# Optimization experiments

Hardware: AMD Instinct MI355X
Metric: run time of the kernel (lower is better)

Reference implementation:

```python
import jax, jax.numpy as jnp
import numpy as np
import math

B, C, T = 4, 512, 2048
LN_EPS = 1e-5

def setup_inputs() -> dict:
    key = jax.random.key(0)
    ks = jax.random.split(key, 12)
    s = 1.0 / math.sqrt(C)
    inp = {
        'feat': jax.random.normal(ks[0], (B, C, T), dtype=jnp.float32),
        'Wq': jax.random.normal(ks[1], (C, C), dtype=jnp.float32) * s,
        'bq': jax.random.normal(ks[2], (C,), dtype=jnp.float32) * s,
        'Wk': jax.random.normal(ks[3], (C, C), dtype=jnp.float32) * s,
        'bk': jax.random.normal(ks[4], (C,), dtype=jnp.float32) * s,
        'Wv': jax.random.normal(ks[5], (C, C), dtype=jnp.float32) * s,
        'bv': jax.random.normal(ks[6], (C,), dtype=jnp.float32) * s,
        'Ws': jax.random.normal(ks[7], (C, C), dtype=jnp.float32) * s,
        'bs': jax.random.normal(ks[8], (C,), dtype=jnp.float32) * s,
        'Wl': jax.random.normal(ks[9], (C,), dtype=jnp.float32) * s,
        'bl': jax.random.normal(ks[10], (1,), dtype=jnp.float32) * s,
    }
    return inp

def reference(feat, Wq, bq, Wk, bk, Wv, bv, Ws, bs, Wl, bl):
    d = feat.shape[1]
    # 1x1 Conv1d == per-position linear over channels. feat: [B,C,T]
    value = jnp.einsum('oc,bct->bto', Wv, feat) + bv          # [B,T,C]
    query = jnp.einsum('oc,bct->bto', Wq, feat) + bq          # [B,T,C]
    key_  = jnp.einsum('oc,bct->bct', Wk, feat) + bk[:, None] # [B,C,T]
    f = jnp.einsum('btc,bcs->bts', query, key_) / math.sqrt(d)
    f = jax.nn.softmax(f, axis=2)                             # [B,T,T]
    y = jnp.einsum('bts,bsc->btc', f, value)                  # [B,T,C]
    f_score = jax.nn.sigmoid(jnp.einsum('btc,c->bt', y, Wl) + bl[0])
    z = jnp.einsum('bts,bsc->btc', 1.0 - f, value)            # [B,T,C]
    b_score = 1.0 - jax.nn.sigmoid(jnp.einsum('btc,c->bt', z, Wl) + bl[0])
    f_score = (f_score + b_score) / 2.0
    y_ct = jnp.einsum('oc,btc->bot', Ws, y) + bs[:, None]     # smooth conv, [B,C,T]
    out = feat + y_ct
    # LayerNorm over (C, T) jointly, default affine (weight=1, bias=0)
    mu = jnp.mean(out, axis=(1, 2), keepdims=True)
    var = jnp.mean(jnp.square(out - mu), axis=(1, 2), keepdims=True)
    out = (out - mu) * jax.lax.rsqrt(var + LN_EPS)
    return out, f_score
```

## Files before the change

### kernel.cpp

```cpp
#include <hip/hip_runtime.h>
#include <hip/hip_bf16.h>

#define BB 4
#define CC 512
#define TT 2048
static constexpr long CT  = (long)CC * TT;
static constexpr long TC  = (long)TT * CC;
static constexpr long TTT = (long)TT * TT;
static constexpr float SM_SCALE = 0.04419417382415922f;

typedef __bf16 bf16;
typedef __attribute__((ext_vector_type(8))) __bf16 bf16x8;
typedef __attribute__((ext_vector_type(4))) __bf16 bf16x4;
typedef __attribute__((ext_vector_type(4))) float f32x4;

__device__ __forceinline__ void load_lds16(const bf16* g, bf16* l)
{
    __builtin_amdgcn_global_load_lds(
        (const __attribute__((address_space(1))) void*)g,
        (__attribute__((address_space(3))) void*)l, 16, 0, 0);
}

template <int TM, int TN, int WR, int WC, int BK>
struct Core {
    static constexpr int THREADS = WR * WC * 64;
    static constexpr int MI = TM / (WR * 16);
    static constexpr int NI = TN / (WC * 16);
    static constexpr int CPR = BK / 8;
    static constexpr int RSH = (BK == 64) ? 3 : 2;
    static constexpr int CMASK = CPR - 1;
    static constexpr int CHUNKS = (TM + TN) * CPR;
    static constexpr int ACH = TM * CPR;
    static constexpr int CPT = CHUNKS / THREADS;
    static_assert(CPT * THREADS == CHUNKS, "chunk divisibility");

    __device__ static __forceinline__ void run(
        const bf16* __restrict__ Ab, const bf16* __restrict__ Bb,
        int K, int m0, int n0, bf16* As, bf16* Bs, f32x4 (&acc)[MI][NI])
    {
        const int tid  = threadIdx.x;
        const int lane = tid & 63;
        const int wid  = tid >> 6;
        const int wr = (wid / WC) * (MI * 16);
        const int wc = (wid % WC) * (NI * 16);
        const int lm = lane & 15;
        const int lq = lane >> 4;
        for (int k0 = 0; k0 < K; k0 += BK) {
#pragma unroll
            for (int i = 0; i < CPT; ++i) {
                int c = tid + i * THREADS;
                if (c < ACH) {
                    int row = c >> RSH;
                    int gc  = (c & CMASK) ^ (row & CMASK);
                    load_lds16(Ab + (long)(m0 + row) * K + k0 + gc * 8, As + c * 8);
                } else {
                    int d = c - ACH;
                    int row = d >> RSH;
                    int gc  = (d & CMASK) ^ (row & CMASK);
                    load_lds16(Bb + (long)(n0 + row) * K + k0 + gc * 8, Bs + d * 8);
                }
            }
            __syncthreads();
#pragma unroll
            for (int ks = 0; ks < BK / 32; ++ks) {
                bf16x8 af[MI], bfr[NI];
#pragma unroll
                for (int i = 0; i < MI; ++i) {
                    int ar = wr + i * 16 + lm;
                    int cc = (ks * 4 + lq) ^ (ar & CMASK);
                    af[i] = *(const bf16x8*)(As + ar * BK + cc * 8);
                }
#pragma unroll
                for (int i = 0; i < NI; ++i) {
                    int br = wc + i * 16 + lm;
                    int cc = (ks * 4 + lq) ^ (br & CMASK);
                    bfr[i] = *(const bf16x8*)(Bs + br * BK + cc * 8);
                }
#pragma unroll
                for (int mi = 0; mi < MI; ++mi)
#pragma unroll
                    for (int ni = 0; ni < NI; ++ni)
                        acc[mi][ni] = __builtin_amdgcn_mfma_f32_16x16x32_bf16(
                            af[mi], bfr[ni], acc[mi][ni], 0, 0, 0);
            }
            __syncthreads();
        }
    }
};

struct CoreQV {
    static constexpr int THREADS = 512;
    static constexpr int MI = 2;
    static constexpr int NI = 4;
    static constexpr int BK = 64;
    static constexpr int CPR = 8, RSH = 3, CMASK = 7;
    static constexpr int ACH = 128 * 8;
    static constexpr int CHUNKS = 256 * 8;
    static constexpr int CPT = CHUNKS / THREADS;

    __device__ static __forceinline__ void run(
        const bf16* __restrict__ Ab, const bf16* __restrict__ Bq,
        const bf16* __restrict__ Bv,
        int m0, bf16* As, bf16* Bs, f32x4 (&acc)[MI][NI])
    {
        const int tid  = threadIdx.x;
        const int lane = tid & 63;
        const int wid  = tid >> 6;
        const int wr = (wid / 2) * 32;
        const int wc = (wid % 2) * 64;
        const int lm = lane & 15;
        const int lq = lane >> 4;
        for (int k0 = 0; k0 < 512; k0 += BK) {
#pragma unroll
            for (int i = 0; i < CPT; ++i) {
                int c = tid + i * THREADS;
                if (c < ACH) {
                    int row = c >> RSH;
                    int gc  = (c & CMASK) ^ (row & CMASK);
                    load_lds16(Ab + (long)(m0 + row) * 512 + k0 + gc * 8, As + c * 8);
                } else {
                    int d = c - ACH;
                    int row = d >> RSH;
                    int gc  = (d & CMASK) ^ (row & CMASK);
                    const bf16* src = (row < 64)
                        ? Bq + (long)row * 512
                        : Bv + (long)(row - 64) * 512;
                    load_lds16(src + k0 + gc * 8, Bs + d * 8);
                }
            }
            __syncthreads();
#pragma unroll
            for (int ks = 0; ks < 2; ++ks) {
                bf16x8 af[MI], bfr[NI];
#pragma unroll
                for (int i = 0; i < MI; ++i) {
                    int ar = wr + i * 16 + lm;
                    int cc = (ks * 4 + lq) ^ (ar & CMASK);
                    af[i] = *(const bf16x8*)(As + ar * BK + cc * 8);
                }
#pragma unroll
                for (int i = 0; i < NI; ++i) {
                    int br = wc + i * 16 + lm;
                    int cc = (ks * 4 + lq) ^ (br & CMASK);
                    bfr[i] = *(const bf16x8*)(Bs + br * BK + cc * 8);
                }
#pragma unroll
                for (int mi = 0; mi < MI; ++mi)
#pragma unroll
                    for (int ni = 0; ni < NI; ++ni)
                        acc[mi][ni] = __builtin_amdgcn_mfma_f32_16x16x32_bf16(
                            af[mi], bfr[ni], acc[mi][ni], 0, 0, 0);
            }
            __syncthreads();
        }
    }
};

__global__ __launch_bounds__(512)
void gemm_qv_kernel(const bf16* __restrict__ featT, const bf16* __restrict__ Wq_bf,
                    const bf16* __restrict__ Wv_bf, bf16* __restrict__ Qb,
                    bf16* __restrict__ Vt, const float* __restrict__ bq,
                    const float* __restrict__ bv, const float* __restrict__ wkc,
                    const float* __restrict__ bk, float* __restrict__ qb)
{
    __shared__ bf16 As[128 * 64];
    __shared__ bf16 Bs[128 * 64];
    const int rb = blockIdx.z;
    const int m0 = blockIdx.y * 128;
    const int ng = blockIdx.x;
    const long wofs = (long)(ng * 64) * 512;
    f32x4 acc[2][4] = {};
    CoreQV::run(featT + (long)rb * TC, Wq_bf + wofs, Wv_bf + wofs, m0, As, Bs, acc);

    const int lane = threadIdx.x & 63, wid = threadIdx.x >> 6;
    const int wr = (wid / 2) * 32;
    const bool isV = wid & 1;
    const int lm = lane & 15, lq = lane >> 4;

    if (isV) {
        bf16* outV = Vt + (long)rb * CT;
#pragma unroll
        for (int mi = 0; mi < 2; ++mi)
#pragma unroll
            for (int ni = 0; ni < 4; ++ni) {
                int n = ng * 64 + ni * 16 + lm;
                float bn = bv[n];
                int mb = m0 + wr + mi * 16 + lq * 4;
                bf16x4 pk;
#pragma unroll
                for (int r = 0; r < 4; ++r) pk[r] = (bf16)(acc[mi][ni][r] + bn);
                *(bf16x4*)(outV + (long)n * TT + mb) = pk;
            }
    } else {
        bf16* out = Qb + (long)rb * TC;
        float* qbb = qb + (long)rb * TT;
        float rs[2][4] = {};
#pragma unroll
        for (int mi = 0; mi < 2; ++mi)
#pragma unroll
            for (int ni = 0; ni < 4; ++ni) {
                int n = ng * 64 + ni * 16 + lm;
                float bn = bq[n], wn = wkc[n], kn = bk[n];
#pragma unroll
                for (int r = 0; r < 4; ++r) {
                    int m = m0 + wr + mi * 16 + lq * 4 + r;
                    float v = acc[mi][ni][r] + bn;
                    rs[mi][r] += v * kn;
                    out[(long)m * 512 + n] = (bf16)(v * wn);
                }
            }
#pragma unroll
        for (int mi = 0; mi < 2; ++mi)
#pragma unroll
            for (int r = 0; r < 4; ++r) {
                float s = rs[mi][r];
                s += __shfl_xor(s, 1, 64); s += __shfl_xor(s, 2, 64);
                s += __shfl_xor(s, 4, 64); s += __shfl_xor(s, 8, 64);
                if (lm == 0)
                    atomicAdd(qbb + m0 + wr + mi * 16 + lq * 4 + r, s);
            }
    }
}

__global__ __launch_bounds__(512, 2)
void gemm_s256_kernel(const bf16* __restrict__ Qb, const bf16* __restrict__ featT,
                      bf16* __restrict__ S, const float* __restrict__ qb,
                      float* __restrict__ rsum)
{
    __shared__ __align__(16) bf16 lds[2][2][256 * 64];
    const int id   = blockIdx.x;
    const int xcd  = id & 7, sIdx = id >> 3;
    const int bz   = xcd >> 1;
    const int n0   = (sIdx & 7) * 256;
    const int m0   = (((xcd & 1) << 2) + (sIdx >> 3)) * 256;
    const bf16* __restrict__ Ab = Qb + (long)bz * TC;
    const bf16* __restrict__ Bb = featT + (long)bz * TC;

    const int tid  = threadIdx.x;
    const int lane = tid & 63;
    const int wid  = tid >> 6;
    const int lm = lane & 15, lq = lane >> 4;
    const int wrb = (wid >> 2) * 64;
    const int wcb = (wid & 3) * 32;

    f32x4 acc[8][4] = {};

#define FENCE asm volatile("" ::: "memory")

#define STAGE_HT(t, op, h)                                                    \
    do {                                                                      \
        const bf16* gp_ = (op) ? Bb : Ab;                                     \
        const int  br_  = ((op) ? n0 : m0) + (h) * 128;                       \
        bf16* lp_ = &lds[(t) & 1][op][(h) * 128 * 64];                        \
        _Pragma("unroll")                                                     \
        for (int i_ = 0; i_ < 2; ++i_) {                                      \
            int c_ = tid + i_ * 512;                                          \
            int r_ = c_ >> 3;                                                 \
            int g_ = (c_ & 7) ^ (r_ & 7);                                     \
            load_lds16(gp_ + (long)(br_ + r_) * 512 + (t) * 64 + g_ * 8,      \
                       lp_ + c_ * 8);                                         \
        }                                                                     \
    } while (0)

#define PHASE(t, qm, qn, doSt, st, sop, sh, doVm)                             \
    do {                                                                      \
        bf16x8 af[2][4], bfr[2][2];                                           \
        const bf16* Al_ = lds[(t) & 1][0];                                    \
        const bf16* Bl_ = lds[(t) & 1][1];                                    \
        _Pragma("unroll")                                                     \
        for (int ks = 0; ks < 2; ++ks) {                                      \
            _Pragma("unroll")                                                 \
            for (int j = 0; j < 4; ++j) {                                     \
                int ar = (qm) * 128 + wrb + j * 16 + lm;                      \
                int cc = (ks * 4 + lq) ^ (ar & 7);                            \
                af[ks][j] = *(const bf16x8*)(Al_ + ar * 64 + cc * 8);         \
            }                                                                 \
            _Pragma("unroll")                                                 \
            for (int j = 0; j < 2; ++j) {                                     \
                int br = (qn) * 128 + wcb + j * 16 + lm;                      \
                int cc = (ks * 4 + lq) ^ (br & 7);                            \
                bfr[ks][j] = *(const bf16x8*)(Bl_ + br * 64 + cc * 8);        \
            }                                                                 \
        }                                                                     \
        if (doSt) STAGE_HT(st, sop, sh);                                      \
        if (doVm) {                                                           \
            if ((t) < 6) asm volatile("s_waitcnt vmcnt(4)" ::: "memory");     \
            else         asm volatile("s_waitcnt vmcnt(0)" ::: "memory");     \
        }                                                                     \
        FENCE; __builtin_amdgcn_s_barrier(); FENCE;                           \
        __builtin_amdgcn_s_setprio(1);                                        \
        _Pragma("unroll")                                                     \
        for (int ks = 0; ks < 2; ++ks)                                        \
            _Pragma("unroll")                                                 \
            for (int j = 0; j < 4; ++j)                                       \
                _Pragma("unroll")                                             \
                for (int j2 = 0; j2 < 2; ++j2)                                \
                    acc[(qm) * 4 + j][(qn) * 2 + j2] =                        \
                        __builtin_amdgcn_mfma_f32_16x16x32_bf16(              \
                            af[ks][j], bfr[ks][j2],                           \
                            acc[(qm) * 4 + j][(qn) * 2 + j2], 0, 0, 0);       \
        __builtin_amdgcn_s_setprio(0);                                        \
        FENCE; __builtin_amdgcn_s_barrier(); FENCE;                           \
    } while (0)

    STAGE_HT(0, 0, 0); STAGE_HT(0, 1, 0); STAGE_HT(0, 0, 1); STAGE_HT(0, 1, 1);
    STAGE_HT(1, 0, 0); STAGE_HT(1, 1, 0);
    asm volatile("s_waitcnt vmcnt(4)" ::: "memory");
    FENCE; __builtin_amdgcn_s_barrier(); FENCE;

    for (int t = 0; t < 8; ++t) {
        PHASE(t, 0, 0, t + 1 < 8, t + 1, 0, 1, false);
        PHASE(t, 0, 1, t + 1 < 8, t + 1, 1, 1, false);
        PHASE(t, 1, 0, t + 2 < 8, t + 2, 0, 0, false);
        PHASE(t, 1, 1, t + 2 < 8, t + 2, 1, 0, true);
    }
#undef PHASE
#undef STAGE_HT
#undef FENCE

    bf16* outp = S + (long)bz * TTT;
    const float* qbb = qb + (long)bz * TT;
    float* rsb = rsum + (long)bz * TT;
#pragma unroll
    for (int mi = 0; mi < 8; ++mi) {
        const int mrow = m0 + (mi >> 2) * 128 + wrb + (mi & 3) * 16 + lq * 4;
        const f32x4 qv = *(const f32x4*)(qbb + mrow);
        float rp[4] = {0.f, 0.f, 0.f, 0.f};
#pragma unroll
        for (int ni = 0; ni < 4; ++ni) {
            const int ncol = n0 + (ni >> 1) * 128 + wcb + (ni & 1) * 16 + lm;
#pragma unroll
            for (int r = 0; r < 4; ++r) {
                float p = __expf((acc[mi][ni][r] + qv[r]) * SM_SCALE);
                outp[(long)(mrow + r) * 2048 + ncol] = (bf16)p;
                rp[r] += p;
            }
        }
#pragma unroll
        for (int r = 0; r < 4; ++r) {
            float s2 = rp[r];
            s2 += __shfl_xor(s2, 1, 64); s2 += __shfl_xor(s2, 2, 64);
            s2 += __shfl_xor(s2, 4, 64); s2 += __shfl_xor(s2, 8, 64);
            if (lm == 0) atomicAdd(rsb + mrow + r, s2);
        }
    }
}

using CY = Core<128, 64, 4, 2, 64>;
__global__ __launch_bounds__(512)
void gemm_y_kernel(const bf16* __restrict__ S, const bf16* __restrict__ Vt,
                   bf16* __restrict__ Yb, const float* __restrict__ Wl,
                   const float* __restrict__ rsum, float* __restrict__ u)
{
    __shared__ bf16 As[128 * 64];
    __shared__ bf16 Bs[64 * 64];
    const int id = blockIdx.x;
    const int xcd = id & 7, s = id >> 3;
    const int rb = xcd >> 1;
    const int n0 = (s & 7) * 64;
    const int m0 = (((xcd & 1) << 3) + (s >> 3)) * 128;
    f32x4 acc[CY::MI][CY::NI] = {};
    CY::run(S + (long)rb * TTT, Vt + (long)rb * CT, 2048, m0, n0, As, Bs, acc);

    const int lane = threadIdx.x & 63, wid = threadIdx.x >> 6;
    const int wr = (wid / 2) * 32, wc = (wid % 2) * 32;
    const int lm = lane & 15, lq = lane >> 4;
    bf16* out = Yb + (long)rb * TC;
    const float* rsb = rsum + (long)rb * TT;
    float* ub = u + (long)rb * TT;
    float inv[2][4];
#pragma unroll
    for (int mi = 0; mi < 2; ++mi)
#pragma unroll
        for (int r = 0; r < 4; ++r)
            inv[mi][r] = 1.f / rsb[m0 + wr + mi * 16 + lq * 4 + r];
    float rs[2][4] = {};
#pragma unroll
    for (int mi = 0; mi < 2; ++mi)
#pragma unroll
        for (int ni = 0; ni < 2; ++ni) {
            int n = n0 + wc + ni * 16 + lm;
            float wn = Wl[n];
#pragma unroll
            for (int r = 0; r < 4; ++r) {
                int m = m0 + wr + mi * 16 + lq * 4 + r;
                float v = acc[mi][ni][r] * inv[mi][r];
                out[(long)m * 512 + n] = (bf16)v;
                rs[mi][r] += v * wn;
            }
        }
#pragma unroll
    for (int mi = 0; mi < 2; ++mi)
#pragma unroll
        for (int r = 0; r < 4; ++r) {
            float s2 = rs[mi][r];
            s2 += __shfl_xor(s2, 1, 64); s2 += __shfl_xor(s2, 2, 64);
            s2 += __shfl_xor(s2, 4, 64); s2 += __shfl_xor(s2, 8, 64);
            if (lm == 0)
                atomicAdd(ub + m0 + wr + mi * 16 + lq * 4 + r, s2);
        }
}

using CF = Core<128, 64, 4, 2, 64>;
__global__ __launch_bounds__(512)
void gemm_final_kernel(const bf16* __restrict__ Yb, const bf16* __restrict__ Ws_bf,
                       float* __restrict__ out, const float* __restrict__ bs,
                       const float* __restrict__ feat, double* __restrict__ stats)
{
    __shared__ bf16 As[128 * 64];
    __shared__ bf16 Bs[64 * 64];
    __shared__ float red[16];
    const int id = blockIdx.x;
    const int xcd = id & 7, s = id >> 3;
    const int bz = xcd >> 1;
    const int n0 = (s & 7) * 64;
    const int m0 = (((xcd & 1) << 3) + (s >> 3)) * 128;
    f32x4 acc[CF::MI][CF::NI] = {};
    CF::run(Yb + (long)bz * TC, Ws_bf, 512, m0, n0, As, Bs, acc);

    const int tid = threadIdx.x;
    const int lane = tid & 63, wid = tid >> 6;
    const int wr = (wid / 2) * 32, wc = (wid % 2) * 32;
    const int lm = lane & 15, lq = lane >> 4;
    float s1 = 0.f, s2 = 0.f;
#pragma unroll
    for (int mi = 0; mi < 2; ++mi)
#pragma unroll
        for (int ni = 0; ni < 2; ++ni) {
            int mbase = m0 + wr + mi * 16 + lq * 4;
            int n = n0 + wc + ni * 16 + lm;
            long off = (long)bz * CT + (long)n * TT + mbase;
            f32x4 fv = *(const f32x4*)(feat + off);
            float bn = bs[n];
            f32x4 res;
#pragma unroll
            for (int r = 0; r < 4; ++r) {
                float v = acc[mi][ni][r] + bn + fv[r];
                res[r] = v;
                s1 += v;
                s2 += v * v;
            }
            *(f32x4*)(out + off) = res;
        }
#pragma unroll
    for (int off = 32; off; off >>= 1) {
        s1 += __shfl_xor(s1, off, 64);
        s2 += __shfl_xor(s2, off, 64);
    }
    if (lane == 0) { red[wid] = s1; red[8 + wid] = s2; }
    __syncthreads();
    if (tid == 0) {
        double t1 = 0.0, t2 = 0.0;
#pragma unroll
        for (int w = 0; w < 8; ++w) { t1 += red[w]; t2 += red[8 + w]; }
        atomicAdd(stats + bz * 2, t1);
        atomicAdd(stats + bz * 2 + 1, t2);
    }
}

__global__ __launch_bounds__(256)
void prep_kernel(const float* __restrict__ feat, bf16* __restrict__ featT,
                 const float* __restrict__ Wq, const float* __restrict__ Wv,
                 const float* __restrict__ Ws, bf16* __restrict__ Wbf,
                 const float* __restrict__ Wk, const float* __restrict__ Wl,
                 const float* __restrict__ bv, float* __restrict__ wkc,
                 float* __restrict__ wvl, float* __restrict__ wlbv,
                 float* __restrict__ frp, float* __restrict__ qb,
                 float* __restrict__ u, float* __restrict__ rsum,
                 double* __restrict__ stats)
{
    const int blk = blockIdx.x;
    const int tid = threadIdx.x;
    if (blk < 4096) {
        __shared__ float tile[32][33];
        __shared__ float sfr[4][32];
        const int b  = blk >> 10;
        const int c0 = ((blk & 1023) >> 6) * 32;
        const int tt = blk & 63;
        const int t0 = tt * 32;
        const int tx = tid & 31;
        const int ty = tid >> 5;
#pragma unroll
        for (int j = 0; j < 4; ++j) {
            int c = c0 + ty + j * 8;
            tile[ty + j * 8][tx] = feat[(long)b * CT + (long)c * TT + t0 + tx];
        }
        __syncthreads();
        float ps = 0.f;
#pragma unroll
        for (int j = 0; j < 4; ++j) {
            int tl = ty + j * 8;
            int t = t0 + tl;
            int c = c0 + tx;
            float v = tile[tx][tl];
            ps += v;
            featT[(long)b * TC + (long)t * CC + c] = (bf16)v;
        }
        const int wid = tid >> 6;
        ps += __shfl_xor(ps, 32, 64);
        if ((tid & 63) < 32) sfr[wid][tx] = ps;
        __syncthreads();
        if (tid < 32) {
            float s = sfr[0][tid] + sfr[1][tid] + sfr[2][tid] + sfr[3][tid];
            frp[(((long)b * 64 + tt) << 9) + c0 + tid] = s;
        }
    } else if (blk < 4480) {
        long gid = (long)(blk - 4096) * 256 + tid;
        long idx = gid * 8;
        int w = (int)(idx >> 18);
        long off = idx & 262143;
        const float* src = (w == 0) ? Wq : (w == 1) ? Wv : Ws;
        f32x4 a = *(const f32x4*)(src + off);
        f32x4 b = *(const f32x4*)(src + off + 4);
        bf16x8 o;
#pragma unroll
        for (int j = 0; j < 4; ++j) { o[j] = (bf16)a[j]; o[4 + j] = (bf16)b[j]; }
        *(bf16x8*)(Wbf + idx) = o;
    } else {
        int mid = (blk - 4480) * 256 + tid;
        if (mid < 512) {
            float s = 0.f;
            for (int o = 0; o < 512; ++o) s += Wk[o * 512 + mid];
            wkc[mid] = s;
        } else if (mid < 1024) {
            int k = mid - 512;
            float s = 0.f;
            for (int c = 0; c < 512; ++c) s += Wl[c] * Wv[c * 512 + k];
            wvl[k] = s;
        } else if (mid < 1088) {
            int lane = mid - 1024;
            float s = 0.f;
#pragma unroll
            for (int j = 0; j < 8; ++j) s += Wl[lane + 64 * j] * bv[lane + 64 * j];
#pragma unroll
            for (int off = 32; off; off >>= 1) s += __shfl_xor(s, off, 64);
            if (lane == 0) wlbv[0] = s;
        } else if (mid >= 1152 && mid < 1160) {
            stats[mid - 1152] = 0.0;
        } else if (mid >= 4096 && mid < 12288) {
            qb[mid - 4096] = 0.f;
        } else if (mid >= 12288 && mid < 20480) {
            u[mid - 12288] = 0.f;
        } else if (mid >= 20480 && mid < 28672) {
            rsum[mid - 20480] = 0.f;
        }
    }
}

__global__ __launch_bounds__(256)
void ln_score_kernel(float* __restrict__ out, const double* __restrict__ stats,
                     const float* __restrict__ u, const float* __restrict__ frp,
                     const float* __restrict__ wvl, const float* __restrict__ wlbv,
                     const float* __restrict__ blp)
{
    if (blockIdx.x < 4096) {
        long i = ((long)blockIdx.x * 256 + threadIdx.x) * 4;
        int b = (int)(i >> 20);
        const double n = 1048576.0;
        double mu  = stats[b * 2] / n;
        double var = stats[b * 2 + 1] / n - mu * mu;
        float rs = (float)(1.0 / sqrt(var + 1e-5));
        float muf = (float)mu;
        f32x4 v = *(f32x4*)(out + i);
#pragma unroll
        for (int j = 0; j < 4; ++j) v[j] = (v[j] - muf) * rs;
        *(f32x4*)(out + i) = v;
    } else {
        const int b = blockIdx.x - 4096;
        __shared__ float ssv[4];
        const int tid = threadIdx.x, lane = tid & 63, wid = tid >> 6;
        const float* fb = frp + ((long)b * 64 << 9);
        float s0 = 0.f, s1 = 0.f;
#pragma unroll 8
        for (int k = 0; k < 64; ++k) {
            s0 += fb[(k << 9) + tid];
            s1 += fb[(k << 9) + tid + 256];
        }
        float p = s0 * wvl[tid] + s1 * wvl[tid + 256];
#pragma unroll
        for (int off = 32; off; off >>= 1) p += __shfl_xor(p, off, 64);
        if (lane == 0) ssv[wid] = p;
        __syncthreads();
        const float sv = ssv[0] + ssv[1] + ssv[2] + ssv[3] + 2048.f * wlbv[0];
        const float bl0 = blp[0];
#pragma unroll
        for (int j = 0; j < 8; ++j) {
            int t = tid + j * 256;
            float uu = u[(long)b * TT + t];
            float uf = uu + bl0;
            float vf = sv - uu + bl0;
            float fs  = 1.f / (1.f + __expf(-uf));
            float bsc = 1.f - 1.f / (1.f + __expf(-vf));
            out[(long)BB * CT + (long)b * TT + t] = 0.5f * (fs + bsc);
        }
    }
}

extern "C" void kernel_launch(void* const* d_in, const int* in_sizes, int n_in,
                              void* d_out, int out_size, void* d_ws, size_t ws_size,
                              hipStream_t stream)
{
    const float* feat = (const float*)d_in[0];
    const float* Wq   = (const float*)d_in[1];
    const float* bq   = (const float*)d_in[2];
    const float* Wk   = (const float*)d_in[3];
    const float* bk   = (const float*)d_in[4];
    const float* Wv   = (const float*)d_in[5];
    const float* bv   = (const float*)d_in[6];
    const float* Ws   = (const float*)d_in[7];
    const float* bs   = (const float*)d_in[8];
    const float* Wl   = (const float*)d_in[9];
    const float* bl   = (const float*)d_in[10];
    float* out = (float*)d_out;

    if (ws_size < 69316736) return;
    char* ws = (char*)d_ws;
    bf16* featT  = (bf16*)(ws);
    bf16* Wbf    = (bf16*)(ws + 8388608);
    bf16* Qb     = (bf16*)(ws + 9961472);
    bf16* Vt     = (bf16*)(ws + 18350080);
    bf16* Yb     = (bf16*)(ws + 26738688);
    bf16* S      = (bf16*)(ws + 35127296);
    float* wkc   = (float*)(ws + 68689920);
    float* wvl   = (float*)(ws + 68691968);
    float* wlbv  = (float*)(ws + 68694016);
    float* qb    = (float*)(ws + 68694080);
    double* stats= (double*)(ws + 68726848);
    float* u     = (float*)(ws + 68726912);
    float* rsum  = (float*)(ws + 68759680);
    float* frp   = (float*)(ws + 68792448);

    bf16* Wq_bf = Wbf;
    bf16* Wv_bf = Wbf + 262144;
    bf16* Ws_bf = Wbf + 524288;

    prep_kernel<<<4592, 256, 0, stream>>>(feat, featT, Wq, Wv, Ws, Wbf, Wk, Wl, bv,
                                          wkc, wvl, wlbv, frp, qb, u, rsum, stats);
    gemm_qv_kernel<<<dim3(8, 16, 4), 512, 0, stream>>>(
        featT, Wq_bf, Wv_bf, Qb, Vt, bq, bv, wkc, bk, qb);
    gemm_s256_kernel<<<256, 512, 0, stream>>>(Qb, featT, S, qb, rsum);
    gemm_y_kernel<<<512, 512, 0, stream>>>(S, Vt, Yb, Wl, rsum, u);
    gemm_final_kernel<<<512, 512, 0, stream>>>(Yb, Ws_bf, out, bs, feat, stats);
    ln_score_kernel<<<4100, 256, 0, stream>>>(out, stats, u, frp, wvl, wlbv, bl);
}
```

Before: 220.5 us.

## Reassociate smoothing conv into value projection and fuse into attention output GEMM

Precomputes V·Wsᵀ with a small GEMM, then multiplies the softmax matrix by it, applying 1/rowsum, bias, residual and LayerNorm stats in that single large GEMM's epilogue. This removes the separate Y = P·V GEMM plus the Y·Ws GEMM and the Yb round trip through memory. The Wl·y score term is now built from per-position V·Wl dot products, accumulated in the S epilogue with extra atomics. The large GEMM uses 128x128 tiles with 256 blocks instead of 128x64 with 512, and the vl scratch buffer reuses the Vpt region.

```diff
diff --git a/kernel.cpp b/kernel.cpp
--- a/kernel.cpp
+++ b/kernel.cpp
@@ -87,6 +87,8 @@
         }
     }
 };
+
+using CO = Core<128, 128, 4, 2, 64>;
 
 struct CoreQV {
     static constexpr int THREADS = 512;
@@ -159,9 +161,10 @@
 __global__ __launch_bounds__(512)
 void gemm_qv_kernel(const bf16* __restrict__ featT, const bf16* __restrict__ Wq_bf,
                     const bf16* __restrict__ Wv_bf, bf16* __restrict__ Qb,
-                    bf16* __restrict__ Vt, const float* __restrict__ bq,
+                    bf16* __restrict__ Vn, const float* __restrict__ bq,
                     const float* __restrict__ bv, const float* __restrict__ wkc,
-                    const float* __restrict__ bk, float* __restrict__ qb)
+                    const float* __restrict__ bk, float* __restrict__ qb,
+                    const float* __restrict__ Wl, float* __restrict__ vl)
 {
     __shared__ bf16 As[128 * 64];
     __shared__ bf16 Bs[128 * 64];
@@ -178,18 +181,32 @@
     const int lm = lane & 15, lq = lane >> 4;
 
     if (isV) {
-        bf16* outV = Vt + (long)rb * CT;
+        bf16* outV = Vn + (long)rb * TC;
+        float* vlb = vl + (long)rb * TT;
+        float vs_[2][4] = {};
 #pragma unroll
         for (int mi = 0; mi < 2; ++mi)
 #pragma unroll
             for (int ni = 0; ni < 4; ++ni) {
                 int n = ng * 64 + ni * 16 + lm;
-                float bn = bv[n];
-                int mb = m0 + wr + mi * 16 + lq * 4;
-                bf16x4 pk;
-#pragma unroll
-                for (int r = 0; r < 4; ++r) pk[r] = (bf16)(acc[mi][ni][r] + bn);
-                *(bf16x4*)(outV + (long)n * TT + mb) = pk;
+                float bn = bv[n], wn = Wl[n];
+#pragma unroll
+                for (int r = 0; r < 4; ++r) {
+                    int m = m0 + wr + mi * 16 + lq * 4 + r;
+                    float v = acc[mi][ni][r] + bn;
+                    outV[(long)m * 512 + n] = (bf16)v;
+                    vs_[mi][r] += v * wn;
+                }
+            }
+#pragma unroll
+        for (int mi = 0; mi < 2; ++mi)
+#pragma unroll
+            for (int r = 0; r < 4; ++r) {
+                float s = vs_[mi][r];
+                s += __shfl_xor(s, 1, 64); s += __shfl_xor(s, 2, 64);
+                s += __shfl_xor(s, 4, 64); s += __shfl_xor(s, 8, 64);
+                if (lm == 0)
+                    atomicAdd(vlb + m0 + wr + mi * 16 + lq * 4 + r, s);
             }
     } else {
         bf16* out = Qb + (long)rb * TC;
@@ -225,7 +242,8 @@
 __global__ __launch_bounds__(512, 2)
 void gemm_s256_kernel(const bf16* __restrict__ Qb, const bf16* __restrict__ featT,
                       bf16* __restrict__ S, const float* __restrict__ qb,
-                      float* __restrict__ rsum)
+                      float* __restrict__ rsum, const float* __restrict__ vl,
+                      float* __restrict__ u)
 {
     __shared__ __align__(16) bf16 lds[2][2][256 * 64];
     const int id   = blockIdx.x;
@@ -320,122 +338,117 @@
 
     bf16* outp = S + (long)bz * TTT;
     const float* qbb = qb + (long)bz * TT;
+    const float* vlb = vl + (long)bz * TT;
     float* rsb = rsum + (long)bz * TT;
+    float* ub  = u + (long)bz * TT;
 #pragma unroll
     for (int mi = 0; mi < 8; ++mi) {
         const int mrow = m0 + (mi >> 2) * 128 + wrb + (mi & 3) * 16 + lq * 4;
         const f32x4 qv = *(const f32x4*)(qbb + mrow);
         float rp[4] = {0.f, 0.f, 0.f, 0.f};
+        float up[4] = {0.f, 0.f, 0.f, 0.f};
 #pragma unroll
         for (int ni = 0; ni < 4; ++ni) {
             const int ncol = n0 + (ni >> 1) * 128 + wcb + (ni & 1) * 16 + lm;
+            const float vlv = vlb[ncol];
 #pragma unroll
             for (int r = 0; r < 4; ++r) {
                 float p = __expf((acc[mi][ni][r] + qv[r]) * SM_SCALE);
                 outp[(long)(mrow + r) * 2048 + ncol] = (bf16)p;
                 rp[r] += p;
+                up[r] += p * vlv;
             }
         }
 #pragma unroll
         for (int r = 0; r < 4; ++r) {
-            float s2 = rp[r];
+            float s2 = rp[r], s3 = up[r];
             s2 += __shfl_xor(s2, 1, 64); s2 += __shfl_xor(s2, 2, 64);
             s2 += __shfl_xor(s2, 4, 64); s2 += __shfl_xor(s2, 8, 64);
-            if (lm == 0) atomicAdd(rsb + mrow + r, s2);
-        }
-    }
-}
-
-using CY = Core<128, 64, 4, 2, 64>;
+            s3 += __shfl_xor(s3, 1, 64); s3 += __shfl_xor(s3, 2, 64);
+            s3 += __shfl_xor(s3, 4, 64); s3 += __shfl_xor(s3, 8, 64);
+            if (lm == 0) {
+                atomicAdd(rsb + mrow + r, s2);
+                atomicAdd(ub + mrow + r, s3);
+            }
+        }
+    }
+}
+
 __global__ __launch_bounds__(512)
-void gemm_y_kernel(const bf16* __restrict__ S, const bf16* __restrict__ Vt,
-                   bf16* __restrict__ Yb, const float* __restrict__ Wl,
-                   const float* __restrict__ rsum, float* __restrict__ u)
+void gemm_vs_kernel(const bf16* __restrict__ Vn, const bf16* __restrict__ Ws_bf,
+                    bf16* __restrict__ Vpt)
 {
     __shared__ bf16 As[128 * 64];
-    __shared__ bf16 Bs[64 * 64];
+    __shared__ bf16 Bs[128 * 64];
     const int id = blockIdx.x;
     const int xcd = id & 7, s = id >> 3;
-    const int rb = xcd >> 1;
-    const int n0 = (s & 7) * 64;
-    const int m0 = (((xcd & 1) << 3) + (s >> 3)) * 128;
-    f32x4 acc[CY::MI][CY::NI] = {};
-    CY::run(S + (long)rb * TTT, Vt + (long)rb * CT, 2048, m0, n0, As, Bs, acc);
+    const int bz = xcd >> 1;
+    const int m0 = (((xcd & 1) << 1) + (s >> 4)) * 128;
+    const int n0 = (s & 15) * 128;
+    f32x4 acc[2][4] = {};
+    CO::run(Ws_bf, Vn + (long)bz * TC, 512, m0, n0, As, Bs, acc);
 
     const int lane = threadIdx.x & 63, wid = threadIdx.x >> 6;
-    const int wr = (wid / 2) * 32, wc = (wid % 2) * 32;
+    const int wr = (wid / 2) * 32, wc = (wid % 2) * 64;
     const int lm = lane & 15, lq = lane >> 4;
-    bf16* out = Yb + (long)rb * TC;
-    const float* rsb = rsum + (long)rb * TT;
-    float* ub = u + (long)rb * TT;
-    float inv[2][4];
+    bf16* out = Vpt + (long)bz * CT;
 #pragma unroll
     for (int mi = 0; mi < 2; ++mi)
 #pragma unroll
-        for (int r = 0; r < 4; ++r)
-            inv[mi][r] = 1.f / rsb[m0 + wr + mi * 16 + lq * 4 + r];
-    float rs[2][4] = {};
-#pragma unroll
-    for (int mi = 0; mi < 2; ++mi)
-#pragma unroll
-        for (int ni = 0; ni < 2; ++ni) {
+        for (int ni = 0; ni < 4; ++ni) {
             int n = n0 + wc + ni * 16 + lm;
-            float wn = Wl[n];
 #pragma unroll
             for (int r = 0; r < 4; ++r) {
                 int m = m0 + wr + mi * 16 + lq * 4 + r;
-                float v = acc[mi][ni][r] * inv[mi][r];
-                out[(long)m * 512 + n] = (bf16)v;
-                rs[mi][r] += v * wn;
-            }
-        }
-#pragma unroll
-    for (int mi = 0; mi < 2; ++mi)
-#pragma unroll
-        for (int r = 0; r < 4; ++r) {
-            float s2 = rs[mi][r];
-            s2 += __shfl_xor(s2, 1, 64); s2 += __shfl_xor(s2, 2, 64);
-            s2 += __shfl_xor(s2, 4, 64); s2 += __shfl_xor(s2, 8, 64);
-            if (lm == 0)
-                atomicAdd(ub + m0 + wr + mi * 16 + lq * 4 + r, s2);
-        }
-}
-
-using CF = Core<128, 64, 4, 2, 64>;
+                out[(long)m * 2048 + n] = (bf16)acc[mi][ni][r];
+            }
+        }
+}
+
 __global__ __launch_bounds__(512)
-void gemm_final_kernel(const bf16* __restrict__ Yb, const bf16* __restrict__ Ws_bf,
-                       float* __restrict__ out, const float* __restrict__ bs,
-                       const float* __restrict__ feat, double* __restrict__ stats)
+void gemm_out_kernel(const bf16* __restrict__ S, const bf16* __restrict__ Vpt,
+                     float* __restrict__ out, const float* __restrict__ bs,
+                     const float* __restrict__ feat,
+                     const float* __restrict__ rsum, double* __restrict__ stats)
 {
     __shared__ bf16 As[128 * 64];
-    __shared__ bf16 Bs[64 * 64];
+    __shared__ bf16 Bs[128 * 64];
     __shared__ float red[16];
     const int id = blockIdx.x;
     const int xcd = id & 7, s = id >> 3;
     const int bz = xcd >> 1;
-    const int n0 = (s & 7) * 64;
-    const int m0 = (((xcd & 1) << 3) + (s >> 3)) * 128;
-    f32x4 acc[CF::MI][CF::NI] = {};
-    CF::run(Yb + (long)bz * TC, Ws_bf, 512, m0, n0, As, Bs, acc);
+    const int n0 = (s & 3) * 128;
+    const int m0 = (((xcd & 1) << 3) + (s >> 2)) * 128;
+    f32x4 acc[2][4] = {};
+    CO::run(S + (long)bz * TTT, Vpt + (long)bz * CT, 2048, m0, n0, As, Bs, acc);
 
     const int tid = threadIdx.x;
     const int lane = tid & 63, wid = tid >> 6;
-    const int wr = (wid / 2) * 32, wc = (wid % 2) * 32;
+    const int wr = (wid / 2) * 32, wc = (wid % 2) * 64;
     const int lm = lane & 15, lq = lane >> 4;
+    const float* rsb = rsum + (long)bz * TT;
+    float inv[2][4];
+#pragma unroll
+    for (int mi = 0; mi < 2; ++mi) {
+        int mrow = m0 + wr + mi * 16 + lq * 4;
+        f32x4 rv = *(const f32x4*)(rsb + mrow);
+#pragma unroll
+        for (int r = 0; r < 4; ++r) inv[mi][r] = 1.f / rv[r];
+    }
     float s1 = 0.f, s2 = 0.f;
 #pragma unroll
     for (int mi = 0; mi < 2; ++mi)
 #pragma unroll
-        for (int ni = 0; ni < 2; ++ni) {
-            int mbase = m0 + wr + mi * 16 + lq * 4;
+        for (int ni = 0; ni < 4; ++ni) {
+            int mrow = m0 + wr + mi * 16 + lq * 4;
             int n = n0 + wc + ni * 16 + lm;
-            long off = (long)bz * CT + (long)n * TT + mbase;
+            long off = (long)bz * CT + (long)n * TT + mrow;
             f32x4 fv = *(const f32x4*)(feat + off);
             float bn = bs[n];
             f32x4 res;
 #pragma unroll
             for (int r = 0; r < 4; ++r) {
-                float v = acc[mi][ni][r] + bn + fv[r];
+                float v = acc[mi][ni][r] * inv[mi][r] + bn + fv[r];
                 res[r] = v;
                 s1 += v;
                 s2 += v * v;
@@ -467,7 +480,7 @@
                  float* __restrict__ wvl, float* __restrict__ wlbv,
                  float* __restrict__ frp, float* __restrict__ qb,
                  float* __restrict__ u, float* __restrict__ rsum,
-                 double* __restrict__ stats)
+                 double* __restrict__ stats, float* __restrict__ vl)
 {
     const int blk = blockIdx.x;
     const int tid = threadIdx.x;
@@ -543,6 +556,8 @@
             u[mid - 12288] = 0.f;
         } else if (mid >= 20480 && mid < 28672) {
             rsum[mid - 20480] = 0.f;
+        } else if (mid >= 28672 && mid < 36864) {
+            vl[mid - 28672] = 0.f;
         }
     }
 }
@@ -551,7 +566,7 @@
 void ln_score_kernel(float* __restrict__ out, const double* __restrict__ stats,
                      const float* __restrict__ u, const float* __restrict__ frp,
                      const float* __restrict__ wvl, const float* __restrict__ wlbv,
-                     const float* __restrict__ blp)
+                     const float* __restrict__ blp, const float* __restrict__ rsum)
 {
     if (blockIdx.x < 4096) {
         long i = ((long)blockIdx.x * 256 + threadIdx.x) * 4;
@@ -586,7 +601,7 @@
 #pragma unroll
         for (int j = 0; j < 8; ++j) {
             int t = tid + j * 256;
-            float uu = u[(long)b * TT + t];
+            float uu = u[(long)b * TT + t] / rsum[(long)b * TT + t];
             float uf = uu + bl0;
             float vf = sv - uu + bl0;
             float fs  = 1.f / (1.f + __expf(-uf));
@@ -618,8 +633,9 @@
     bf16* featT  = (bf16*)(ws);
     bf16* Wbf    = (bf16*)(ws + 8388608);
     bf16* Qb     = (bf16*)(ws + 9961472);
-    bf16* Vt     = (bf16*)(ws + 18350080);
-    bf16* Yb     = (bf16*)(ws + 26738688);
+    bf16* Vn     = (bf16*)(ws + 18350080);
+    bf16* Vpt    = (bf16*)(ws + 26738688);
+    float* vl    = (float*)(ws + 26738688);
     bf16* S      = (bf16*)(ws + 35127296);
     float* wkc   = (float*)(ws + 68689920);
     float* wvl   = (float*)(ws + 68691968);
@@ -634,12 +650,12 @@
     bf16* Wv_bf = Wbf + 262144;
     bf16* Ws_bf = Wbf + 524288;
 
-    prep_kernel<<<4592, 256, 0, stream>>>(feat, featT, Wq, Wv, Ws, Wbf, Wk, Wl, bv,
-                                          wkc, wvl, wlbv, frp, qb, u, rsum, stats);
+    prep_kernel<<<4624, 256, 0, stream>>>(feat, featT, Wq, Wv, Ws, Wbf, Wk, Wl, bv,
+                                          wkc, wvl, wlbv, frp, qb, u, rsum, stats, vl);
     gemm_qv_kernel<<<dim3(8, 16, 4), 512, 0, stream>>>(
-        featT, Wq_bf, Wv_bf, Qb, Vt, bq, bv, wkc, bk, qb);
-    gemm_s256_kernel<<<256, 512, 0, stream>>>(Qb, featT, S, qb, rsum);
-    gemm_y_kernel<<<512, 512, 0, stream>>>(S, Vt, Yb, Wl, rsum, u);
-    gemm_final_kernel<<<512, 512, 0, stream>>>(Yb, Ws_bf, out, bs, feat, stats);
-    ln_score_kernel<<<4100, 256, 0, stream>>>(out, stats, u, frp, wvl, wlbv, bl);
-}
+        featT, Wq_bf, Wv_bf, Qb, Vn, bq, bv, wkc, bk, qb, Wl, vl);
+    gemm_s256_kernel<<<256, 512, 0, stream>>>(Qb, featT, S, qb, rsum, vl, u);
+    gemm_vs_kernel<<<256, 512, 0, stream>>>(Vn, Ws_bf, Vpt);
+    gemm_out_kernel<<<256, 512, 0, stream>>>(S, Vpt, out, bs, feat, rsum, stats);
+    ln_score_kernel<<<4100, 256, 0, stream>>>(out, stats, u, frp, wvl, wlbv, bl, rsum);
+}
```

Result: no change. 222.1 us (+0.7%).
